# Optimization experiments

Hardware: AMD Instinct MI355X
Metric: run time of the kernel (lower is better)

## Reference

```python
import jax, jax.numpy as jnp
import numpy as np

N = 8192
D_IN = 60
NUM_CLASSES = 10


def _xavier(key, out_f, in_f):
    limit = float(np.sqrt(6.0 / (in_f + out_f)))
    return jax.random.uniform(key, (out_f, in_f), jnp.float32, -limit, limit)


def setup_inputs() -> dict:
    key = jax.random.key(0)
    ks = jax.random.split(key, 10)
    return {
        "x": jax.random.normal(ks[0], (N, D_IN), jnp.float32),
        "fc1_w": _xavier(ks[1], 32, 60),
        "fc1_b": jnp.zeros((32,), jnp.float32),
        "fc2_w": _xavier(ks[2], 16, 32),
        "fc2_b": jnp.zeros((16,), jnp.float32),
        "fc3_w": _xavier(ks[3], 8, 60),
        "fc3_b": jnp.zeros((8,), jnp.float32),
        "fc6_w": _xavier(ks[4], NUM_CLASSES, 8),
        "fc6_b": jnp.zeros((NUM_CLASSES,), jnp.float32),
        "temp": jnp.float32(1.0) + 0.1 * jax.random.truncated_normal(ks[5], -2.0, 2.0, (), jnp.float32),
        "theta": jnp.float32(1.0) + 0.1 * jax.random.truncated_normal(ks[6], -2.0, 2.0, (), jnp.float32),
    }


def _pairwise_sq_dist(z):
    # z: [N, d] -> [N, N] squared euclidean distances, clamped at 0
    sq = jnp.sum(z * z, axis=1)  # [N]
    dist = sq[:, None] + sq[None, :] - 2.0 * (z @ z.T)
    return jnp.maximum(dist, 0.0)


def reference(x, fc1_w, fc1_b, fc2_w, fc2_b, fc3_w, fc3_b, fc6_w, fc6_b, temp, theta):
    net = x @ fc1_w.T + fc1_b           # [N, 32]
    net = net @ fc2_w.T + fc2_b         # [N, 16]
    A = -_pairwise_sq_dist(net)         # [N, N]
    A = jax.nn.sigmoid(temp * A + theta)
    # A * (1 - I) + I == set diagonal to 1
    A = jnp.fill_diagonal(A, 1.0, inplace=False)
    A = A / jnp.sum(A, axis=1, keepdims=True)
    h = A @ x                           # [N, 60] dense graph aggregation
    h = h @ fc3_w.T + fc3_b             # [N, 8]
    return jax.nn.softmax(h @ fc6_w.T + fc6_b, axis=1)  # [N, num_classes]
```

## Files before the change

### kernel.cpp

```cpp
#include <hip/hip_runtime.h>
#include <math.h>

#define NROWS 8192
#define DIN   60
#define DZ    16
#define NC    10

#define LOG2E 1.4426950408889634f

#define RB  256
#define CJ  256
#define NRB (NROWS / RB)
#define NCH (NROWS / CJ)

typedef short bf16x8 __attribute__((ext_vector_type(8)));
typedef float f32x4  __attribute__((ext_vector_type(4)));

__device__ __forceinline__ unsigned int bfr(float f) {
    return (__float_as_uint(f) + 0x8000u) >> 16;
}

__global__ __launch_bounds__(64) void k1_all(
    const float* __restrict__ x,
    const float* __restrict__ w1, const float* __restrict__ b1,
    const float* __restrict__ w2, const float* __restrict__ b2,
    const float* __restrict__ temp_p, const float* __restrict__ theta_p,
    unsigned short* __restrict__ zb, float* __restrict__ bbf,
    unsigned short* __restrict__ xT)
{
    int i = blockIdx.x * 64 + threadIdx.x;

    float xr[DIN];
    const float4* xp = reinterpret_cast<const float4*>(x + (size_t)i * DIN);
    #pragma unroll
    for (int c = 0; c < 15; ++c) {
        float4 v = xp[c];
        xr[c*4+0] = v.x; xr[c*4+1] = v.y; xr[c*4+2] = v.z; xr[c*4+3] = v.w;
    }

    float n1[32];
    #pragma unroll
    for (int o = 0; o < 32; ++o) {
        float acc = b1[o];
        #pragma unroll
        for (int k = 0; k < DIN; ++k) acc = fmaf(w1[o*DIN+k], xr[k], acc);
        n1[o] = acc;
    }

    float z[DZ];
    float sq = 0.0f;
    #pragma unroll
    for (int u = 0; u < DZ; ++u) {
        float acc = b2[u];
        #pragma unroll
        for (int o = 0; o < 32; ++o) acc = fmaf(w2[u*32+o], n1[o], acc);
        z[u] = acc;
        sq = fmaf(acc, acc, sq);
    }

    float temp  = *temp_p;
    float theta = *theta_p;
    float s = sqrtf(2.0f * temp * LOG2E);

    unsigned int p[8];
    #pragma unroll
    for (int u = 0; u < 8; ++u) {
        unsigned int lo = bfr(z[2*u]   * s);
        unsigned int hi = bfr(z[2*u+1] * s);
        p[u] = lo | (hi << 16);
    }
    uint4* dst = reinterpret_cast<uint4*>(zb + (size_t)i * 32);
    dst[0] = make_uint4(p[0], p[1], p[2], p[3]);
    dst[1] = make_uint4(p[4], p[5], p[6], p[7]);
    dst[2] = make_uint4(0, 0, 0, 0);
    dst[3] = make_uint4(0, 0, 0, 0);

    bbf[i] = LOG2E * fmaf(temp, sq, -0.5f * theta);

    #pragma unroll
    for (int c = 0; c < DIN; ++c)
        xT[(size_t)c * NROWS + i] = (unsigned short)bfr(xr[c]);
    xT[(size_t)60 * NROWS + i] = 0x3F80;
    xT[(size_t)61 * NROWS + i] = 0;
    xT[(size_t)62 * NROWS + i] = 0;
    xT[(size_t)63 * NROWS + i] = 0;
}

__global__ __launch_bounds__(512, 4) void k2_mfma(
    const unsigned short* __restrict__ zb, const float* __restrict__ bbf,
    const unsigned short* __restrict__ xT, const float* __restrict__ theta_p,
    float* __restrict__ hacc)
{
    __shared__ unsigned long long sP[8 * 320];

    const int tid  = threadIdx.x;
    const int lane = tid & 63, wave = tid >> 6;
    const int q = lane & 15, g = lane >> 4;
    const int rb = blockIdx.x & (NRB - 1);
    const int ch = blockIdx.x >> 5;
    const int i0 = rb * RB + wave * 32;
    const int j0 = ch * CJ;

    bf16x8 zbi[2];
    float  bi[2];
    #pragma unroll
    for (int t = 0; t < 2; ++t) {
        zbi[t] = *reinterpret_cast<const bf16x8*>(zb + (size_t)(i0 + t*16 + q) * 32 + g*8);
        bi[t]  = bbf[i0 + t*16 + q];
    }
    const float nclamp = -(*theta_p) * LOG2E;
    const f32x4 z4 = {0.0f, 0.0f, 0.0f, 0.0f};

    f32x4 H[2][4];
    #pragma unroll
    for (int t = 0; t < 2; ++t)
        #pragma unroll
        for (int nt = 0; nt < 4; ++nt) H[t][nt] = z4;

    unsigned long long* myP = sP + wave * 320;

    for (int jp = 0; jp < CJ / 32; ++jp) {
        #pragma unroll
        for (int half = 0; half < 2; ++half) {
            const int gj = j0 + jp*32 + half*16;
            bf16x8 za = *reinterpret_cast<const bf16x8*>(zb + (size_t)(gj + q) * 32 + g*8);
            f32x4  bj = *reinterpret_cast<const f32x4*>(bbf + gj + 4*g);
            #pragma unroll
            for (int t = 0; t < 2; ++t) {
                f32x4 S = __builtin_amdgcn_mfma_f32_16x16x32_bf16(za, zbi[t], z4, 0, 0, 0);
                unsigned int ur[4];
                #pragma unroll
                for (int r = 0; r < 4; ++r) {
                    float n = (bi[t] + bj[r]) - S[r];
                    n = fmaxf(n, nclamp);
                    float P = __builtin_amdgcn_rcpf(1.0f + __builtin_amdgcn_exp2f(n));
                    if (i0 + t*16 == gj && q == 4*g + r) P = 0.0f;
                    ur[r] = __float_as_uint(P) + 0x8000u;
                }
                unsigned int pk0 = (ur[0] >> 16) | (ur[1] & 0xFFFF0000u);
                unsigned int pk1 = (ur[2] >> 16) | (ur[3] & 0xFFFF0000u);
                myP[t*160 + q*10 + half*4 + g] =
                    ((unsigned long long)pk1 << 32) | pk0;
            }
        }
        __syncthreads();

        const int jb = j0 + jp*32;
        bf16x8 pa[2];
        #pragma unroll
        for (int t = 0; t < 2; ++t) {
            union { unsigned long long u[2]; bf16x8 v; } pu;
            pu.u[0] = myP[t*160 + q*10 + g*2];
            pu.u[1] = myP[t*160 + q*10 + g*2 + 1];
            pa[t] = pu.v;
        }
        #pragma unroll
        for (int nt = 0; nt < 4; ++nt) {
            bf16x8 xb = *reinterpret_cast<const bf16x8*>(
                xT + (size_t)(nt*16 + q) * NROWS + jb + g*8);
            H[0][nt] = __builtin_amdgcn_mfma_f32_16x16x32_bf16(pa[0], xb, H[0][nt], 0, 0, 0);
            H[1][nt] = __builtin_amdgcn_mfma_f32_16x16x32_bf16(pa[1], xb, H[1][nt], 0, 0, 0);
        }
        __syncthreads();
    }

    #pragma unroll
    for (int t = 0; t < 2; ++t)
        #pragma unroll
        for (int nt = 0; nt < 4; ++nt)
            #pragma unroll
            for (int r = 0; r < 4; ++r) {
                int row = i0 + t*16 + 4*g + r;
                hacc[((size_t)ch * NROWS + row) * 64 + nt*16 + q] = H[t][nt][r];
            }
}

__global__ __launch_bounds__(256) void k3_reduce(float* __restrict__ hacc)
{
    const int tid = threadIdx.x;
    const int r   = blockIdx.x * 16 + (tid >> 4);
    const int c   = (tid & 15) * 4;

    float4 s = make_float4(0.0f, 0.0f, 0.0f, 0.0f);
    #pragma unroll 8
    for (int ch = 0; ch < NCH; ++ch) {
        float4 v = *reinterpret_cast<const float4*>(
            hacc + ((size_t)ch * NROWS + r) * 64 + c);
        s.x += v.x; s.y += v.y; s.z += v.z; s.w += v.w;
    }
    *reinterpret_cast<float4*>(hacc + (size_t)r * 64 + c) = s;
}

__global__ __launch_bounds__(64) void k3_head(
    const float* __restrict__ x,
    const float* __restrict__ w3, const float* __restrict__ b3,
    const float* __restrict__ w6, const float* __restrict__ b6,
    const float* __restrict__ hacc,
    float* __restrict__ out)
{
    int i = blockIdx.x * 64 + threadIdx.x;

    const float* hi = hacc + (size_t)i * 64;
    const float* xi = x + (size_t)i * DIN;

    float rd = __builtin_amdgcn_rcpf(hi[60] + 1.0f);

    float h[DIN];
    #pragma unroll
    for (int k = 0; k < DIN; ++k) h[k] = (hi[k] + xi[k]) * rd;

    float g[8];
    #pragma unroll
    for (int o = 0; o < 8; ++o) {
        float a = b3[o];
        #pragma unroll
        for (int k = 0; k < DIN; ++k) a = fmaf(w3[o*DIN+k], h[k], a);
        g[o] = a;
    }

    float l[NC];
    float m = -3.0e38f;
    #pragma unroll
    for (int c = 0; c < NC; ++c) {
        float a = b6[c];
        #pragma unroll
        for (int o = 0; o < 8; ++o) a = fmaf(w6[c*8+o], g[o], a);
        l[c] = a;
        m = fmaxf(m, a);
    }
    float e[NC];
    float sum = 0.0f;
    #pragma unroll
    for (int c = 0; c < NC; ++c) {
        e[c] = __builtin_amdgcn_exp2f((l[c] - m) * LOG2E);
        sum += e[c];
    }
    float rsum = __builtin_amdgcn_rcpf(sum);
    #pragma unroll
    for (int c = 0; c < NC; ++c) out[(size_t)i * NC + c] = e[c] * rsum;
}

extern "C" void kernel_launch(void* const* d_in, const int* in_sizes, int n_in,
                              void* d_out, int out_size, void* d_ws, size_t ws_size,
                              hipStream_t stream)
{
    const float* x     = (const float*)d_in[0];
    const float* w1    = (const float*)d_in[1];
    const float* b1    = (const float*)d_in[2];
    const float* w2    = (const float*)d_in[3];
    const float* b2    = (const float*)d_in[4];
    const float* w3    = (const float*)d_in[5];
    const float* b3    = (const float*)d_in[6];
    const float* w6    = (const float*)d_in[7];
    const float* b6    = (const float*)d_in[8];
    const float* temp  = (const float*)d_in[9];
    const float* theta = (const float*)d_in[10];
    float* out = (float*)d_out;

    char* p = (char*)d_ws;
    unsigned short* zbuf = (unsigned short*)p;  p += (size_t)NROWS * 32 * 2;
    float*          bbf  = (float*)p;           p += (size_t)NROWS * 4;
    unsigned short* xT   = (unsigned short*)p;  p += (size_t)64 * NROWS * 2;
    float*          hbuf = (float*)p;

    k1_all  <<<NROWS / 64, 64, 0, stream>>>(x, w1, b1, w2, b2, temp, theta, zbuf, bbf, xT);
    k2_mfma <<<NRB * NCH, 512, 0, stream>>>(zbuf, bbf, xT, theta, hbuf);
    k3_reduce<<<NROWS / 16, 256, 0, stream>>>(hbuf);
    k3_head <<<NROWS / 64, 64, 0, stream>>>(x, w3, b3, w6, b6, hbuf, out);
}
```

Measured before the change: 181.8 us.

## Retile pairwise kernel, drop block barriers, store partials in register-native layout

```diff
diff --git a/kernel.cpp b/kernel.cpp
--- a/kernel.cpp
+++ b/kernel.cpp
@@ -8,10 +8,11 @@
 
 #define LOG2E 1.4426950408889634f
 
-#define RB  256
-#define CJ  256
-#define NRB (NROWS / RB)
-#define NCH (NROWS / CJ)
+#define RB    128
+#define CJ    512
+#define NRB   (NROWS / RB)
+#define NCH   (NROWS / CJ)
+#define WAVES 4
 
 typedef short bf16x8 __attribute__((ext_vector_type(8)));
 typedef float f32x4  __attribute__((ext_vector_type(4)));
@@ -86,18 +87,18 @@
     xT[(size_t)63 * NROWS + i] = 0;
 }
 
-__global__ __launch_bounds__(512, 4) void k2_mfma(
+__global__ __launch_bounds__(256, 4) void k2_mfma(
     const unsigned short* __restrict__ zb, const float* __restrict__ bbf,
     const unsigned short* __restrict__ xT, const float* __restrict__ theta_p,
     float* __restrict__ hacc)
 {
-    __shared__ unsigned long long sP[8 * 320];
+    __shared__ unsigned long long sP[WAVES * 320];
 
     const int tid  = threadIdx.x;
     const int lane = tid & 63, wave = tid >> 6;
     const int q = lane & 15, g = lane >> 4;
     const int rb = blockIdx.x & (NRB - 1);
-    const int ch = blockIdx.x >> 5;
+    const int ch = blockIdx.x >> 6;
     const int i0 = rb * RB + wave * 32;
     const int j0 = ch * CJ;
 
@@ -143,7 +144,7 @@
                     ((unsigned long long)pk1 << 32) | pk0;
             }
         }
-        __syncthreads();
+        __threadfence_block();
 
         const int jb = j0 + jp*32;
         bf16x8 pa[2];
@@ -161,46 +162,54 @@
             H[0][nt] = __builtin_amdgcn_mfma_f32_16x16x32_bf16(pa[0], xb, H[0][nt], 0, 0, 0);
             H[1][nt] = __builtin_amdgcn_mfma_f32_16x16x32_bf16(pa[1], xb, H[1][nt], 0, 0, 0);
         }
-        __syncthreads();
-    }
-
+    }
+
+    float* regout = hacc + (((size_t)(ch * NRB + rb) * WAVES + wave) * 32) * 64;
     #pragma unroll
     for (int t = 0; t < 2; ++t)
         #pragma unroll
         for (int nt = 0; nt < 4; ++nt)
             #pragma unroll
-            for (int r = 0; r < 4; ++r) {
-                int row = i0 + t*16 + 4*g + r;
-                hacc[((size_t)ch * NROWS + row) * 64 + nt*16 + q] = H[t][nt][r];
-            }
-}
-
-__global__ __launch_bounds__(256) void k3_reduce(float* __restrict__ hacc)
-{
-    const int tid = threadIdx.x;
-    const int r   = blockIdx.x * 16 + (tid >> 4);
-    const int c   = (tid & 15) * 4;
-
+            for (int r = 0; r < 4; ++r)
+                regout[(t*16 + nt*4 + r) * 64 + lane] = H[t][nt][r];
+}
+
+#define CHSTRIDE4 (NROWS * 16)
+
+__global__ __launch_bounds__(256) void k3_reduce(
+    const float* __restrict__ hacc, float* __restrict__ hfin)
+{
+    const int T = blockIdx.x * 256 + threadIdx.x;
+
+    const float4* src = reinterpret_cast<const float4*>(hacc) + T;
     float4 s = make_float4(0.0f, 0.0f, 0.0f, 0.0f);
     #pragma unroll 8
     for (int ch = 0; ch < NCH; ++ch) {
-        float4 v = *reinterpret_cast<const float4*>(
-            hacc + ((size_t)ch * NROWS + r) * 64 + c);
+        float4 v = src[(size_t)ch * CHSTRIDE4];
         s.x += v.x; s.y += v.y; s.z += v.z; s.w += v.w;
     }
-    *reinterpret_cast<float4*>(hacc + (size_t)r * 64 + c) = s;
+
+    const int f    = T * 4;
+    const int lane = f & 63;
+    const int slot = (f >> 6) & 31;
+    const int wv   = (f >> 11) & 3;
+    const int rb   = f >> 13;
+    const int i  = rb * RB + wv * 32 + ((slot >> 4) * 16) + ((lane >> 4) * 4) + (slot & 3);
+    const int c0 = ((slot >> 2) & 3) * 16 + (lane & 15);
+
+    *reinterpret_cast<float4*>(hfin + (size_t)i * 64 + c0) = s;
 }
 
 __global__ __launch_bounds__(64) void k3_head(
     const float* __restrict__ x,
     const float* __restrict__ w3, const float* __restrict__ b3,
     const float* __restrict__ w6, const float* __restrict__ b6,
-    const float* __restrict__ hacc,
+    const float* __restrict__ hfin,
     float* __restrict__ out)
 {
     int i = blockIdx.x * 64 + threadIdx.x;
 
-    const float* hi = hacc + (size_t)i * 64;
+    const float* hi = hfin + (size_t)i * 64;
     const float* xi = x + (size_t)i * DIN;
 
     float rd = __builtin_amdgcn_rcpf(hi[60] + 1.0f);
@@ -261,10 +270,11 @@
     unsigned short* zbuf = (unsigned short*)p;  p += (size_t)NROWS * 32 * 2;
     float*          bbf  = (float*)p;           p += (size_t)NROWS * 4;
     unsigned short* xT   = (unsigned short*)p;  p += (size_t)64 * NROWS * 2;
-    float*          hbuf = (float*)p;
-
-    k1_all  <<<NROWS / 64, 64, 0, stream>>>(x, w1, b1, w2, b2, temp, theta, zbuf, bbf, xT);
-    k2_mfma <<<NRB * NCH, 512, 0, stream>>>(zbuf, bbf, xT, theta, hbuf);
-    k3_reduce<<<NROWS / 16, 256, 0, stream>>>(hbuf);
-    k3_head <<<NROWS / 64, 64, 0, stream>>>(x, w3, b3, w6, b6, hbuf, out);
-}
+    float*          hacc = (float*)p;           p += (size_t)NCH * NROWS * 64 * 4;
+    float*          hfin = (float*)p;
+
+    k1_all   <<<NROWS / 64, 64, 0, stream>>>(x, w1, b1, w2, b2, temp, theta, zbuf, bbf, xT);
+    k2_mfma  <<<NRB * NCH, 256, 0, stream>>>(zbuf, bbf, xT, theta, hacc);
+    k3_reduce<<<NROWS * 16 / 256, 256, 0, stream>>>(hacc, hfin);
+    k3_head  <<<NROWS / 64, 64, 0, stream>>>(x, w3, b3, w6, b6, hfin, out);
+}
```

After: 173.5 us. 4.6% less time.

## Shrink per-wave tiles, drop block barriers, fuse reduce with head

Applied to the files above, without the earlier changes.

```diff
diff --git a/kernel.cpp b/kernel.cpp
--- a/kernel.cpp
+++ b/kernel.cpp
@@ -8,10 +8,11 @@
 
 #define LOG2E 1.4426950408889634f
 
-#define RB  256
-#define CJ  256
-#define NRB (NROWS / RB)
-#define NCH (NROWS / CJ)
+#define RB    64
+#define CJ    512
+#define NRB   (NROWS / RB)
+#define NCH   (NROWS / CJ)
+#define WAVES 4
 
 typedef short bf16x8 __attribute__((ext_vector_type(8)));
 typedef float f32x4  __attribute__((ext_vector_type(4)));
@@ -86,38 +87,31 @@
     xT[(size_t)63 * NROWS + i] = 0;
 }
 
-__global__ __launch_bounds__(512, 4) void k2_mfma(
+__global__ __launch_bounds__(256, 8) void k2_mfma(
     const unsigned short* __restrict__ zb, const float* __restrict__ bbf,
     const unsigned short* __restrict__ xT, const float* __restrict__ theta_p,
     float* __restrict__ hacc)
 {
-    __shared__ unsigned long long sP[8 * 320];
+    __shared__ unsigned long long sP[WAVES * 160];
 
     const int tid  = threadIdx.x;
     const int lane = tid & 63, wave = tid >> 6;
     const int q = lane & 15, g = lane >> 4;
     const int rb = blockIdx.x & (NRB - 1);
-    const int ch = blockIdx.x >> 5;
-    const int i0 = rb * RB + wave * 32;
+    const int ch = blockIdx.x >> 7;
+    const int i0 = rb * RB + wave * 16;
     const int j0 = ch * CJ;
 
-    bf16x8 zbi[2];
-    float  bi[2];
-    #pragma unroll
-    for (int t = 0; t < 2; ++t) {
-        zbi[t] = *reinterpret_cast<const bf16x8*>(zb + (size_t)(i0 + t*16 + q) * 32 + g*8);
-        bi[t]  = bbf[i0 + t*16 + q];
-    }
+    bf16x8 zbi = *reinterpret_cast<const bf16x8*>(zb + (size_t)(i0 + q) * 32 + g*8);
+    float  bi  = bbf[i0 + q];
     const float nclamp = -(*theta_p) * LOG2E;
     const f32x4 z4 = {0.0f, 0.0f, 0.0f, 0.0f};
 
-    f32x4 H[2][4];
-    #pragma unroll
-    for (int t = 0; t < 2; ++t)
-        #pragma unroll
-        for (int nt = 0; nt < 4; ++nt) H[t][nt] = z4;
-
-    unsigned long long* myP = sP + wave * 320;
+    f32x4 H[4];
+    #pragma unroll
+    for (int nt = 0; nt < 4; ++nt) H[nt] = z4;
+
+    unsigned long long* myP = sP + wave * 160;
 
     for (int jp = 0; jp < CJ / 32; ++jp) {
         #pragma unroll
@@ -125,119 +119,117 @@
             const int gj = j0 + jp*32 + half*16;
             bf16x8 za = *reinterpret_cast<const bf16x8*>(zb + (size_t)(gj + q) * 32 + g*8);
             f32x4  bj = *reinterpret_cast<const f32x4*>(bbf + gj + 4*g);
+            f32x4 S = __builtin_amdgcn_mfma_f32_16x16x32_bf16(za, zbi, z4, 0, 0, 0);
+            unsigned int ur[4];
             #pragma unroll
-            for (int t = 0; t < 2; ++t) {
-                f32x4 S = __builtin_amdgcn_mfma_f32_16x16x32_bf16(za, zbi[t], z4, 0, 0, 0);
-                unsigned int ur[4];
-                #pragma unroll
-                for (int r = 0; r < 4; ++r) {
-                    float n = (bi[t] + bj[r]) - S[r];
-                    n = fmaxf(n, nclamp);
-                    float P = __builtin_amdgcn_rcpf(1.0f + __builtin_amdgcn_exp2f(n));
-                    if (i0 + t*16 == gj && q == 4*g + r) P = 0.0f;
-                    ur[r] = __float_as_uint(P) + 0x8000u;
-                }
-                unsigned int pk0 = (ur[0] >> 16) | (ur[1] & 0xFFFF0000u);
-                unsigned int pk1 = (ur[2] >> 16) | (ur[3] & 0xFFFF0000u);
-                myP[t*160 + q*10 + half*4 + g] =
-                    ((unsigned long long)pk1 << 32) | pk0;
+            for (int r = 0; r < 4; ++r) {
+                float n = (bi + bj[r]) - S[r];
+                n = fmaxf(n, nclamp);
+                float P = __builtin_amdgcn_rcpf(1.0f + __builtin_amdgcn_exp2f(n));
+                if (i0 == gj && q == 4*g + r) P = 0.0f;
+                ur[r] = __float_as_uint(P) + 0x8000u;
             }
-        }
-        __syncthreads();
+            unsigned int pk0 = (ur[0] >> 16) | (ur[1] & 0xFFFF0000u);
+            unsigned int pk1 = (ur[2] >> 16) | (ur[3] & 0xFFFF0000u);
+            myP[q*10 + half*4 + g] = ((unsigned long long)pk1 << 32) | pk0;
+        }
+        __threadfence_block();
 
         const int jb = j0 + jp*32;
-        bf16x8 pa[2];
-        #pragma unroll
-        for (int t = 0; t < 2; ++t) {
+        bf16x8 pa;
+        {
             union { unsigned long long u[2]; bf16x8 v; } pu;
-            pu.u[0] = myP[t*160 + q*10 + g*2];
-            pu.u[1] = myP[t*160 + q*10 + g*2 + 1];
-            pa[t] = pu.v;
+            pu.u[0] = myP[q*10 + g*2];
+            pu.u[1] = myP[q*10 + g*2 + 1];
+            pa = pu.v;
         }
         #pragma unroll
         for (int nt = 0; nt < 4; ++nt) {
             bf16x8 xb = *reinterpret_cast<const bf16x8*>(
                 xT + (size_t)(nt*16 + q) * NROWS + jb + g*8);
-            H[0][nt] = __builtin_amdgcn_mfma_f32_16x16x32_bf16(pa[0], xb, H[0][nt], 0, 0, 0);
-            H[1][nt] = __builtin_amdgcn_mfma_f32_16x16x32_bf16(pa[1], xb, H[1][nt], 0, 0, 0);
-        }
-        __syncthreads();
-    }
-
-    #pragma unroll
-    for (int t = 0; t < 2; ++t)
-        #pragma unroll
-        for (int nt = 0; nt < 4; ++nt)
-            #pragma unroll
-            for (int r = 0; r < 4; ++r) {
-                int row = i0 + t*16 + 4*g + r;
-                hacc[((size_t)ch * NROWS + row) * 64 + nt*16 + q] = H[t][nt][r];
-            }
-}
-
-__global__ __launch_bounds__(256) void k3_reduce(float* __restrict__ hacc)
-{
-    const int tid = threadIdx.x;
-    const int r   = blockIdx.x * 16 + (tid >> 4);
-    const int c   = (tid & 15) * 4;
-
-    float4 s = make_float4(0.0f, 0.0f, 0.0f, 0.0f);
-    #pragma unroll 8
-    for (int ch = 0; ch < NCH; ++ch) {
-        float4 v = *reinterpret_cast<const float4*>(
-            hacc + ((size_t)ch * NROWS + r) * 64 + c);
-        s.x += v.x; s.y += v.y; s.z += v.z; s.w += v.w;
-    }
-    *reinterpret_cast<float4*>(hacc + (size_t)r * 64 + c) = s;
-}
-
-__global__ __launch_bounds__(64) void k3_head(
+            H[nt] = __builtin_amdgcn_mfma_f32_16x16x32_bf16(pa, xb, H[nt], 0, 0, 0);
+        }
+    }
+
+    float* regout = hacc + (((size_t)(ch * NRB + rb) * WAVES + wave) * 16) * 64;
+    #pragma unroll
+    for (int nt = 0; nt < 4; ++nt)
+        #pragma unroll
+        for (int r = 0; r < 4; ++r)
+            regout[(nt*4 + r) * 64 + lane] = H[nt][r];
+}
+
+__global__ __launch_bounds__(256) void k3_fused(
+    const float* __restrict__ hacc,
     const float* __restrict__ x,
     const float* __restrict__ w3, const float* __restrict__ b3,
     const float* __restrict__ w6, const float* __restrict__ b6,
-    const float* __restrict__ hacc,
     float* __restrict__ out)
 {
-    int i = blockIdx.x * 64 + threadIdx.x;
-
-    const float* hi = hacc + (size_t)i * 64;
-    const float* xi = x + (size_t)i * DIN;
-
-    float rd = __builtin_amdgcn_rcpf(hi[60] + 1.0f);
-
-    float h[DIN];
-    #pragma unroll
-    for (int k = 0; k < DIN; ++k) h[k] = (hi[k] + xi[k]) * rd;
-
-    float g[8];
-    #pragma unroll
-    for (int o = 0; o < 8; ++o) {
-        float a = b3[o];
-        #pragma unroll
-        for (int k = 0; k < DIN; ++k) a = fmaf(w3[o*DIN+k], h[k], a);
-        g[o] = a;
-    }
-
-    float l[NC];
-    float m = -3.0e38f;
-    #pragma unroll
-    for (int c = 0; c < NC; ++c) {
-        float a = b6[c];
-        #pragma unroll
-        for (int o = 0; o < 8; ++o) a = fmaf(w6[c*8+o], g[o], a);
-        l[c] = a;
-        m = fmaxf(m, a);
-    }
-    float e[NC];
-    float sum = 0.0f;
-    #pragma unroll
-    for (int c = 0; c < NC; ++c) {
-        e[c] = __builtin_amdgcn_exp2f((l[c] - m) * LOG2E);
-        sum += e[c];
-    }
-    float rsum = __builtin_amdgcn_rcpf(sum);
-    #pragma unroll
-    for (int c = 0; c < NC; ++c) out[(size_t)i * NC + c] = e[c] * rsum;
+    __shared__ float sh[16][64];
+
+    const int tid = threadIdx.x;
+    const int b   = blockIdx.x;
+
+    {
+        const float4* src = reinterpret_cast<const float4*>(
+            hacc + (size_t)b * 1024) + tid;
+        float4 s = make_float4(0.0f, 0.0f, 0.0f, 0.0f);
+        #pragma unroll 8
+        for (int ch = 0; ch < NCH; ++ch) {
+            float4 v = src[(size_t)ch * (NRB * WAVES * 16 * 64 / 4)];
+            s.x += v.x; s.y += v.y; s.z += v.z; s.w += v.w;
+        }
+        const int f    = tid * 4;
+        const int lane = f & 63;
+        const int slot = (f >> 6) & 15;
+        const int il   = (lane >> 4) * 4 + (slot & 3);
+        const int cl   = ((slot >> 2) & 3) * 16 + (lane & 15);
+        *reinterpret_cast<float4*>(&sh[il][cl]) = s;
+    }
+    __syncthreads();
+
+    if (tid < 16) {
+        const int row = b * 16 + tid;
+        const float* hi = sh[tid];
+        const float* xi = x + (size_t)row * DIN;
+
+        float rd = __builtin_amdgcn_rcpf(hi[60] + 1.0f);
+
+        float h[DIN];
+        #pragma unroll
+        for (int k = 0; k < DIN; ++k) h[k] = (hi[k] + xi[k]) * rd;
+
+        float g[8];
+        #pragma unroll
+        for (int o = 0; o < 8; ++o) {
+            float a = b3[o];
+            #pragma unroll
+            for (int k = 0; k < DIN; ++k) a = fmaf(w3[o*DIN+k], h[k], a);
+            g[o] = a;
+        }
+
+        float l[NC];
+        float m = -3.0e38f;
+        #pragma unroll
+        for (int c = 0; c < NC; ++c) {
+            float a = b6[c];
+            #pragma unroll
+            for (int o = 0; o < 8; ++o) a = fmaf(w6[c*8+o], g[o], a);
+            l[c] = a;
+            m = fmaxf(m, a);
+        }
+        float e[NC];
+        float sum = 0.0f;
+        #pragma unroll
+        for (int c = 0; c < NC; ++c) {
+            e[c] = __builtin_amdgcn_exp2f((l[c] - m) * LOG2E);
+            sum += e[c];
+        }
+        float rsum = __builtin_amdgcn_rcpf(sum);
+        #pragma unroll
+        for (int c = 0; c < NC; ++c) out[(size_t)row * NC + c] = e[c] * rsum;
+    }
 }
 
 extern "C" void kernel_launch(void* const* d_in, const int* in_sizes, int n_in,
@@ -261,10 +253,9 @@
     unsigned short* zbuf = (unsigned short*)p;  p += (size_t)NROWS * 32 * 2;
     float*          bbf  = (float*)p;           p += (size_t)NROWS * 4;
     unsigned short* xT   = (unsigned short*)p;  p += (size_t)64 * NROWS * 2;
-    float*          hbuf = (float*)p;
+    float*          hacc = (float*)p;
 
     k1_all  <<<NROWS / 64, 64, 0, stream>>>(x, w1, b1, w2, b2, temp, theta, zbuf, bbf, xT);
-    k2_mfma <<<NRB * NCH, 512, 0, stream>>>(zbuf, bbf, xT, theta, hbuf);
-    k3_reduce<<<NROWS / 16, 256, 0, stream>>>(hbuf);
-    k3_head <<<NROWS / 64, 64, 0, stream>>>(x, w3, b3, w6, b6, hbuf, out);
-}
+    k2_mfma <<<NRB * NCH, 256, 0, stream>>>(zbuf, bbf, xT, theta, hacc);
+    k3_fused<<<NROWS / 16, 256, 0, stream>>>(hacc, x, w3, b3, w6, b6, out);
+}
```

Result: slower. 208.5 us (+14.7%).
